# Kernel optimization log

Hardware: AMD Instinct MI355X
Metric: run time of the kernel (lower is better)

## Reference

```python
import jax, jax.numpy as jnp
import numpy as np

NEG_SLOPE_GAT = 0.2   # PyG GATConv default negative_slope
NEG_SLOPE_ACT = 0.01  # torch F.leaky_relu default


def gat_conv(x, src, dst, W, att_src, att_dst, b, N):
    # Single-head PyG GATConv with self-loops already appended in (src, dst).
    xl = x @ W                              # [N, d]
    a_src = xl @ att_src                    # [N]
    a_dst = xl @ att_dst                    # [N]
    e = jax.nn.leaky_relu(a_src[src] + a_dst[dst], NEG_SLOPE_GAT)  # [E]
    m = jax.ops.segment_max(e, dst, num_segments=N)                # per-dst max
    ex = jnp.exp(e - m[dst])
    s = jax.ops.segment_sum(ex, dst, num_segments=N)
    alpha = ex / (s[dst] + 1e-16)                                  # softmax over in-edges
    out = jax.ops.segment_sum(alpha[:, None] * xl[src], dst, num_segments=N)
    return out + b


def setup_inputs() -> dict:
    key = jax.random.key(0)
    ks = jax.random.split(key, 10)
    N, E, d_in, h1, h2 = 100000, 1600000, 128, 128, 64
    x = jax.random.normal(ks[0], (N, d_in), dtype=jnp.float32)
    edge_index = jax.random.randint(ks[1], (2, E), 0, N, dtype=jnp.int64)
    s1 = 1.0 / np.sqrt(d_in)
    s2 = 1.0 / np.sqrt(h1)
    W1 = jax.random.uniform(ks[2], (d_in, h1), jnp.float32, -s1, s1)
    att_src1 = jax.random.uniform(ks[3], (h1,), jnp.float32, -s2, s2)
    att_dst1 = jax.random.uniform(ks[4], (h1,), jnp.float32, -s2, s2)
    b1 = jnp.zeros((h1,), jnp.float32)
    s3 = 1.0 / np.sqrt(h2)
    W2 = jax.random.uniform(ks[5], (h1, h2), jnp.float32, -s2, s2)
    att_src2 = jax.random.uniform(ks[6], (h2,), jnp.float32, -s3, s3)
    att_dst2 = jax.random.uniform(ks[7], (h2,), jnp.float32, -s3, s3)
    b2 = jnp.zeros((h2,), jnp.float32)
    return {"x": x, "edge_index": edge_index, "W1": W1, "att_src1": att_src1,
            "att_dst1": att_dst1, "b1": b1, "W2": W2, "att_src2": att_src2,
            "att_dst2": att_dst2, "b2": b2}


def reference(x, edge_index, W1, att_src1, att_dst1, b1, W2, att_src2, att_dst2, b2):
    N = x.shape[0]
    loops = jnp.arange(N, dtype=edge_index.dtype)
    src = jnp.concatenate([edge_index[0], loops])  # add self-loops (PyG default)
    dst = jnp.concatenate([edge_index[1], loops])
    h = gat_conv(x, src, dst, W1, att_src1, att_dst1, b1, N)
    h = jax.nn.leaky_relu(h, NEG_SLOPE_ACT)
    # dropout omitted (deterministic reference / eval mode)
    h = gat_conv(h, src, dst, W2, att_src2, att_dst2, b2, N)
    return jax.nn.softmax(h, axis=0)
```

## Files before the change

### kernel.cpp

```cpp
#include <hip/hip_runtime.h>
#include <hip/hip_fp16.h>
#include <math.h>


constexpr int NPARTS = 256;
constexpr int PCAP = 8192;
constexpr int CHUNK = 4096;
constexpr int DPPMAX = 400;

typedef _Float16 f16x8 __attribute__((ext_vector_type(8)));
typedef float f32x4 __attribute__((ext_vector_type(4)));

__global__ __launch_bounds__(256) void k_part(
    const int* __restrict__ srcA, const int* __restrict__ dstA,
    int* __restrict__ pcur, uint2* __restrict__ parts,
    int* __restrict__ ovf, int* __restrict__ ovf_cnt,
    int E, int N, int DPP, int nch, int ovfcap) {
  __shared__ int hist[NPARTS];
  __shared__ int base[NPARTS];
  const int tot = E + N;
  for (int c = blockIdx.x; c < nch; c += gridDim.x) {
    hist[threadIdx.x] = 0;
    __syncthreads();
    const int beg = c * CHUNK;
    int pp[16], rr[16], ss[16], dd[16];
#pragma unroll
    for (int j = 0; j < 16; ++j) {
      int e = beg + j * 256 + (int)threadIdx.x;
      int d = -1, s = 0;
      if (e < tot) {
        if (e < E) { d = dstA[e]; s = srcA[e]; } else { d = s = e - E; }
      }
      dd[j] = d; ss[j] = s;
      int p = (d >= 0) ? (d / DPP) : -1;
      pp[j] = p;
      rr[j] = (p >= 0) ? atomicAdd(&hist[p], 1) : 0;
    }
    __syncthreads();
    base[threadIdx.x] = atomicAdd(&pcur[threadIdx.x], hist[threadIdx.x]);
    __syncthreads();
#pragma unroll
    for (int j = 0; j < 16; ++j) {
      int p = pp[j];
      if (p < 0) continue;
      int pos = base[p] + rr[j];
      if (pos < PCAP) {
        parts[(size_t)p * PCAP + pos] = make_uint2((unsigned)ss[j], (unsigned)dd[j]);
      } else {
        int o = atomicAdd(ovf_cnt, 1);
        if (o < ovfcap) { ovf[2 * o] = dd[j]; ovf[2 * o + 1] = ss[j]; }
      }
    }
    __syncthreads();
  }
}

__global__ __launch_bounds__(256) void k_pscan(const int* __restrict__ pcur,
                                               int* __restrict__ pbase) {
  __shared__ int sc[NPARTS];
  int t = threadIdx.x;
  int v = min(pcur[t], PCAP);
  sc[t] = v;
  __syncthreads();
  for (int o = 1; o < NPARTS; o <<= 1) {
    int x = (t >= o) ? sc[t - o] : 0;
    __syncthreads();
    sc[t] += x;
    __syncthreads();
  }
  pbase[t + 1] = sc[t];
  if (t == 0) pbase[0] = 0;
}

__global__ __launch_bounds__(256) void k_place(
    const uint2* __restrict__ parts, const int* __restrict__ pbase,
    int* __restrict__ rowptr, int* __restrict__ seidx,
    int N, int DPP, int nparts) {
  __shared__ int l_cnt[DPPMAX];
  __shared__ int l_off[DPPMAX];
  __shared__ int l_out[PCAP];
  const int p = blockIdx.x;
  const int t = threadIdx.x;
  const int d0 = p * DPP;
  const int ndst = min(DPP, N - d0);
  const int base = pbase[p];
  const int n = pbase[p + 1] - base;
  const uint2* pe = parts + (size_t)p * PCAP;

  for (int i = t; i < ndst; i += 256) l_cnt[i] = 0;
  __syncthreads();
  for (int i = t; i < n; i += 256) {
    uint2 e = pe[i];
    atomicAdd(&l_cnt[(int)e.y - d0], 1);
  }
  __syncthreads();
  if (t == 0) {
    int run = 0;
    for (int i = 0; i < ndst; ++i) { l_off[i] = run; run += l_cnt[i]; }
  }
  __syncthreads();
  for (int i = t; i < ndst; i += 256) {
    rowptr[d0 + i] = base + l_off[i];
    l_cnt[i] = l_off[i];
  }
  if (p == nparts - 1 && t == 0) rowptr[N] = base + n;
  __syncthreads();
  for (int i = t; i < n; i += 256) {
    uint2 e = pe[i];
    int pos = atomicAdd(&l_cnt[(int)e.y - d0], 1);
    l_out[pos] = (int)e.x;
  }
  __syncthreads();
  for (int i = t; i < n; i += 256)
    seidx[base + i] = l_out[i];
}

__global__ __launch_bounds__(256) void k_wprep(
    const float* __restrict__ W1, const float* __restrict__ W2,
    _Float16* __restrict__ Wf1, _Float16* __restrict__ Wf2) {
  int t = blockIdx.x * blockDim.x + threadIdx.x;
  int stride = gridDim.x * blockDim.x;
  for (int i = t; i < 8 * 4 * 64 * 8; i += stride) {
    int j = i & 7, l = (i >> 3) & 63, kk = (i >> 9) & 3, cb = i >> 11;
    int k = kk * 32 + (l >> 4) * 8 + j, c = cb * 16 + (l & 15);
    Wf1[i] = (_Float16)W1[k * 128 + c];
  }
  for (int i = t; i < 4 * 4 * 64 * 8; i += stride) {
    int j = i & 7, l = (i >> 3) & 63, kk = (i >> 9) & 3, cb = i >> 11;
    int k = kk * 32 + (l >> 4) * 8 + j, c = cb * 16 + (l & 15);
    Wf2[i] = (_Float16)W2[k * 64 + c];
  }
}

template <int C>
__device__ __forceinline__ void gemm_mfma_body(
    const float* __restrict__ X, const _Float16* __restrict__ Wf,
    const float* __restrict__ atts, const float* __restrict__ attd,
    __half* __restrict__ XLh, float* __restrict__ a_s, float* __restrict__ a_d,
    int N) {
  constexpr int NCB = C / 16;
  const int lane = threadIdx.x & 63;
  const int wv = threadIdx.x >> 6;
  const int r0 = blockIdx.x * 64 + wv * 16;
  const int arow = lane & 15;
  const int grp = lane >> 4;
  const int r = r0 + arow;
  const int rsafe = (r < N) ? r : (N - 1);

  float av[NCB], dv[NCB];
#pragma unroll
  for (int cb = 0; cb < NCB; ++cb) {
    av[cb] = atts[cb * 16 + arow];
    dv[cb] = attd[cb * 16 + arow];
  }

  f16x8 af[4];
  const float* xr = X + (size_t)rsafe * 128 + grp * 8;
#pragma unroll
  for (int kk = 0; kk < 4; ++kk) {
    float4 u0 = *(const float4*)(xr + kk * 32);
    float4 u1 = *(const float4*)(xr + kk * 32 + 4);
    af[kk][0] = (_Float16)u0.x; af[kk][1] = (_Float16)u0.y;
    af[kk][2] = (_Float16)u0.z; af[kk][3] = (_Float16)u0.w;
    af[kk][4] = (_Float16)u1.x; af[kk][5] = (_Float16)u1.y;
    af[kk][6] = (_Float16)u1.z; af[kk][7] = (_Float16)u1.w;
  }

  float ps[4] = {0.f, 0.f, 0.f, 0.f};
  float pd[4] = {0.f, 0.f, 0.f, 0.f};

#pragma unroll
  for (int cb = 0; cb < NCB; ++cb) {
    f32x4 acc = {0.f, 0.f, 0.f, 0.f};
#pragma unroll
    for (int kk = 0; kk < 4; ++kk) {
      f16x8 bf = *(const f16x8*)(Wf + ((size_t)(cb * 4 + kk) * 64 + lane) * 8);
      acc = __builtin_amdgcn_mfma_f32_16x16x32_f16(af[kk], bf, acc, 0, 0, 0);
    }
    const int ocol = cb * 16 + arow;
#pragma unroll
    for (int i = 0; i < 4; ++i) {
      const int orow = r0 + grp * 4 + i;
      if (orow < N) XLh[(size_t)orow * C + ocol] = (__half)(_Float16)acc[i];
      ps[i] = fmaf(acc[i], av[cb], ps[i]);
      pd[i] = fmaf(acc[i], dv[cb], pd[i]);
    }
  }
#pragma unroll
  for (int m = 1; m < 16; m <<= 1) {
#pragma unroll
    for (int i = 0; i < 4; ++i) {
      ps[i] += __shfl_xor(ps[i], m);
      pd[i] += __shfl_xor(pd[i], m);
    }
  }
  if (arow == 0) {
#pragma unroll
    for (int i = 0; i < 4; ++i) {
      const int orow = r0 + grp * 4 + i;
      if (orow < N) { a_s[orow] = ps[i]; a_d[orow] = pd[i]; }
    }
  }
}

__global__ __launch_bounds__(256) void k_gemm_l1(
    const float* __restrict__ X, const _Float16* __restrict__ Wf,
    const float* __restrict__ atts, const float* __restrict__ attd,
    __half* __restrict__ XLh, float* __restrict__ a_s, float* __restrict__ a_d,
    int N) {
  gemm_mfma_body<128>(X, Wf, atts, attd, XLh, a_s, a_d, N);
}
__global__ __launch_bounds__(256) void k_gemm_l2(
    const float* __restrict__ X, const _Float16* __restrict__ Wf,
    const float* __restrict__ atts, const float* __restrict__ attd,
    __half* __restrict__ XLh, float* __restrict__ a_s, float* __restrict__ a_d,
    int N) {
  gemm_mfma_body<64>(X, Wf, atts, attd, XLh, a_s, a_d, N);
}

template <int C, bool RELU>
__device__ __forceinline__ void aggr_body(
    const __half* __restrict__ XLh, const float* __restrict__ as_,
    const float* __restrict__ ad_, const int* __restrict__ rowptr,
    const int* __restrict__ seidx, const int* __restrict__ ovf,
    const int* __restrict__ ovf_cnt, const float* __restrict__ bias,
    float* __restrict__ OUT, int N) {
  constexpr int PL = C / 64;
  const int lane = threadIdx.x & 63;
  const int wid = threadIdx.x >> 6;
  const int novf = *ovf_cnt;
  float bb[PL];
#pragma unroll
  for (int j = 0; j < PL; ++j) bb[j] = bias[lane * PL + j];

  for (int d = blockIdx.x * 4 + wid; d < N; d += gridDim.x * 4) {
    const int beg = rowptr[d], end = rowptr[d + 1];
    const int nb = end - beg;
    const float adst = ad_[d];

    float s;
    int sv = 0; float ev = 0.f;
    if (nb <= 64) {
      if (lane < nb) {
        sv = seidx[beg + lane];
        float t = as_[sv] + adst;
        t = t > 0.f ? t : 0.2f * t;
        ev = __expf(t);
      }
      s = ev;
    } else {
      s = 0.f;
      for (int i = beg + lane; i < end; i += 64) {
        int s2 = seidx[i];
        float t = as_[s2] + adst;
        t = t > 0.f ? t : 0.2f * t;
        s += __expf(t);
      }
    }
#pragma unroll
    for (int o = 32; o; o >>= 1) s += __shfl_xor(s, o);

    if (novf > 0) {
      float so = 0.f;
      for (int i = lane; i < novf; i += 64) {
        if (ovf[2 * i] == d) {
          float t = as_[ovf[2 * i + 1]] + adst;
          t = t > 0.f ? t : 0.2f * t;
          so += __expf(t);
        }
      }
#pragma unroll
      for (int o = 32; o; o >>= 1) so += __shfl_xor(so, o);
      s += so;
    }
    const float inv = 1.f / (s + 1e-16f);

    float acc[PL];
#pragma unroll
    for (int j = 0; j < PL; ++j) acc[j] = 0.f;

    if (nb <= 64) {
      const float wv = ev * inv;
      auto body = [&](int j) {
        int sj = __shfl(sv, j);
        float wj = __shfl(wv, j);
        if (PL == 2) {
          __half2 hv = *(const __half2*)(XLh + (size_t)sj * C + lane * 2);
          float2 xv = __half22float2(hv);
          acc[0] = fmaf(wj, xv.x, acc[0]);
          acc[1] = fmaf(wj, xv.y, acc[1]);
        } else {
          acc[0] = fmaf(wj, __half2float(XLh[(size_t)sj * C + lane]), acc[0]);
        }
      };
      int j = 0;
      for (; j + 4 <= nb; j += 4) { body(j); body(j + 1); body(j + 2); body(j + 3); }
      for (; j < nb; ++j) body(j);
    } else {
      for (int i0 = beg; i0 < end; i0 += 64) {
        const int nc = min(64, end - i0);
        int sc = 0; float wc = 0.f;
        if (lane < nc) {
          sc = seidx[i0 + lane];
          float t = as_[sc] + adst;
          t = t > 0.f ? t : 0.2f * t;
          wc = __expf(t) * inv;
        }
        for (int j = 0; j < nc; ++j) {
          int sj = __shfl(sc, j);
          float wj = __shfl(wc, j);
          if (PL == 2) {
            __half2 hv = *(const __half2*)(XLh + (size_t)sj * C + lane * 2);
            float2 xv = __half22float2(hv);
            acc[0] = fmaf(wj, xv.x, acc[0]);
            acc[1] = fmaf(wj, xv.y, acc[1]);
          } else {
            acc[0] = fmaf(wj, __half2float(XLh[(size_t)sj * C + lane]), acc[0]);
          }
        }
      }
    }

    if (novf > 0) {
      for (int i = 0; i < novf; ++i) {
        int od = ovf[2 * i];
        if (od != d) continue;
        int os = ovf[2 * i + 1];
        float t = as_[os] + adst;
        t = t > 0.f ? t : 0.2f * t;
        float wj = __expf(t) * inv;
        if (PL == 2) {
          __half2 hv = *(const __half2*)(XLh + (size_t)os * C + lane * 2);
          float2 xv = __half22float2(hv);
          acc[0] = fmaf(wj, xv.x, acc[0]);
          acc[1] = fmaf(wj, xv.y, acc[1]);
        } else {
          acc[0] = fmaf(wj, __half2float(XLh[(size_t)os * C + lane]), acc[0]);
        }
      }
    }

    float o0 = acc[0] + bb[0];
    if (RELU) o0 = o0 > 0.f ? o0 : 0.01f * o0;
    if (PL == 2) {
      float o1 = acc[1] + bb[1];
      if (RELU) o1 = o1 > 0.f ? o1 : 0.01f * o1;
      *(float2*)&OUT[(size_t)d * C + lane * 2] = make_float2(o0, o1);
    } else {
      OUT[(size_t)d * C + lane] = o0;
    }
  }
}

__global__ __launch_bounds__(256) void k_aggr_l1(
    const __half* __restrict__ XLh, const float* __restrict__ as_,
    const float* __restrict__ ad_, const int* __restrict__ rowptr,
    const int* __restrict__ seidx, const int* __restrict__ ovf,
    const int* __restrict__ ovf_cnt, const float* __restrict__ bias,
    float* __restrict__ OUT, int N) {
  aggr_body<128, true>(XLh, as_, ad_, rowptr, seidx, ovf, ovf_cnt, bias, OUT, N);
}
__global__ __launch_bounds__(256) void k_aggr_l2(
    const __half* __restrict__ XLh, const float* __restrict__ as_,
    const float* __restrict__ ad_, const int* __restrict__ rowptr,
    const int* __restrict__ seidx, const int* __restrict__ ovf,
    const int* __restrict__ ovf_cnt, const float* __restrict__ bias,
    float* __restrict__ OUT, int N) {
  aggr_body<64, false>(XLh, as_, ad_, rowptr, seidx, ovf, ovf_cnt, bias, OUT, N);
}

__global__ void k_colsum(const float* __restrict__ O, float* __restrict__ csum, int N) {
  __shared__ float sm[4][64];
  int c = threadIdx.x & 63;
  int wv = threadIdx.x >> 6;
  float s = 0.f;
  for (int r = blockIdx.x * 4 + wv; r < N; r += gridDim.x * 4)
    s += __expf(O[(size_t)r * 64 + c]);
  sm[wv][c] = s;
  __syncthreads();
  if (threadIdx.x < 64) {
    float s2 = sm[0][c] + sm[1][c] + sm[2][c] + sm[3][c];
    atomicAdd(&csum[c], s2);
  }
}

__global__ void k_norm(float* __restrict__ O, const float* __restrict__ csum, size_t tot4) {
  for (size_t i = blockIdx.x * (size_t)blockDim.x + threadIdx.x; i < tot4;
       i += (size_t)gridDim.x * blockDim.x) {
    float4 v = ((float4*)O)[i];
    int c0 = (int)((i * 4) & 63);
    float s0 = csum[c0],     s1 = csum[c0 + 1];
    float s2 = csum[c0 + 2], s3 = csum[c0 + 3];
    v.x = __expf(v.x) / s0;
    v.y = __expf(v.y) / s1;
    v.z = __expf(v.z) / s2;
    v.w = __expf(v.w) / s3;
    ((float4*)O)[i] = v;
  }
}

extern "C" void kernel_launch(void* const* d_in, const int* in_sizes, int n_in,
                              void* d_out, int out_size, void* d_ws, size_t ws_size,
                              hipStream_t stream) {
  const float* x   = (const float*)d_in[0];
  const int*   ei  = (const int*)d_in[1];
  const float* W1  = (const float*)d_in[2];
  const float* as1 = (const float*)d_in[3];
  const float* ad1 = (const float*)d_in[4];
  const float* b1  = (const float*)d_in[5];
  const float* W2  = (const float*)d_in[6];
  const float* as2 = (const float*)d_in[7];
  const float* ad2 = (const float*)d_in[8];
  const float* b2  = (const float*)d_in[9];
  float* out = (float*)d_out;

  const int N = in_sizes[0] / 128;
  const int E = in_sizes[1] / 2;
  const int Etot = E + N;
  const int* srcA = ei;
  const int* dstA = ei + E;
  const int DPP = (N + NPARTS - 1) / NPARTS;
  const int nparts = (N + DPP - 1) / DPP;

  char* w = (char*)d_ws;
  auto take = [&](size_t bytes) -> void* {
    void* p = (void*)w;
    w += (bytes + 255) & ~(size_t)255;
    return p;
  };
  __half*    xlh   = (__half*)take((size_t)N * 128 * 2);
  __half*    xl2h  = (__half*)take((size_t)N * 64 * 2);
  float*     h     = (float*)take((size_t)N * 128 * 4);
  float*     a_s   = (float*)take((size_t)N * 4);
  float*     a_d   = (float*)take((size_t)N * 4);
  int*       zeroB = (int*)take((size_t)(1 + 64 + NPARTS) * 4);
  int*       ovf_cnt = zeroB;
  float*     csum    = (float*)(zeroB + 1);
  int*       pcur    = zeroB + 1 + 64;
  int*       pbase  = (int*)take((size_t)(NPARTS + 1) * 4);
  int*       rowptr = (int*)take((size_t)(N + 1) * 4);
  int*       seidx  = (int*)take((size_t)Etot * 4);
  int*       ovf    = (int*)take((size_t)Etot * 2 * 4);
  uint2*     parts  = (uint2*)take((size_t)NPARTS * PCAP * 8);
  _Float16*  wf1    = (_Float16*)take((size_t)8 * 4 * 64 * 8 * 2);
  _Float16*  wf2    = (_Float16*)take((size_t)4 * 4 * 64 * 8 * 2);

  hipMemsetAsync(zeroB, 0, (size_t)(1 + 64 + NPARTS) * 4, stream);

  const int nch = (Etot + CHUNK - 1) / CHUNK;
  k_part<<<nch, 256, 0, stream>>>(srcA, dstA, pcur, parts, ovf, ovf_cnt,
                                  E, N, DPP, nch, Etot);
  k_wprep<<<32, 256, 0, stream>>>(W1, W2, wf1, wf2);
  k_pscan<<<1, NPARTS, 0, stream>>>(pcur, pbase);
  k_place<<<nparts, 256, 0, stream>>>(parts, pbase, rowptr, seidx, N, DPP, nparts);

  const int gb = (N + 63) / 64;
  k_gemm_l1<<<gb, 256, 0, stream>>>(x, wf1, as1, ad1, xlh, a_s, a_d, N);
  k_aggr_l1<<<8192, 256, 0, stream>>>(xlh, a_s, a_d, rowptr, seidx, ovf, ovf_cnt, b1, h, N);
  k_gemm_l2<<<gb, 256, 0, stream>>>(h, wf2, as2, ad2, xl2h, a_s, a_d, N);
  k_aggr_l2<<<8192, 256, 0, stream>>>(xl2h, a_s, a_d, rowptr, seidx, ovf, ovf_cnt, b2, out, N);

  k_colsum<<<1024, 256, 0, stream>>>(out, csum, N);
  const size_t tot4 = (size_t)N * 64 / 4;
  k_norm<<<2048, 256, 0, stream>>>(out, csum, tot4);
}
```

Measured before the change: 268.6 us.

## Fuse graph build, weight prep, scan/place with GEMM, and colsum into aggregation

Merges the partitioning and weight-conversion kernels into one launch, folds the prefix scan and CSR placement into the layer-1 GEMM launch as extra blocks, and fuses the column exp-sum into a specialized layer-2 aggregation that processes two edges per step with half-waves. Broadcasts use readlane instead of shuffles. Column sums are spread over 8 replicas to cut atomic contention. This reduces launch count and removes a full pass over the output, at the cost of larger shared-memory footprint in the fused GEMM kernel, which may lower its occupancy.

```diff
diff --git a/kernel.cpp b/kernel.cpp
--- a/kernel.cpp
+++ b/kernel.cpp
@@ -11,124 +11,69 @@
 typedef _Float16 f16x8 __attribute__((ext_vector_type(8)));
 typedef float f32x4 __attribute__((ext_vector_type(4)));
 
-__global__ __launch_bounds__(256) void k_part(
+__device__ __forceinline__ int bcasti(int v, int j) {
+  return __builtin_amdgcn_readlane(v, j);
+}
+__device__ __forceinline__ float bcastf(float v, int j) {
+  return __uint_as_float((unsigned)__builtin_amdgcn_readlane((int)__float_as_uint(v), j));
+}
+
+__global__ __launch_bounds__(256) void k_build1(
     const int* __restrict__ srcA, const int* __restrict__ dstA,
     int* __restrict__ pcur, uint2* __restrict__ parts,
     int* __restrict__ ovf, int* __restrict__ ovf_cnt,
+    const float* __restrict__ W1, const float* __restrict__ W2,
+    _Float16* __restrict__ Wf1, _Float16* __restrict__ Wf2,
     int E, int N, int DPP, int nch, int ovfcap) {
+  if ((int)blockIdx.x >= nch) {
+    int t = ((int)blockIdx.x - nch) * 256 + (int)threadIdx.x;
+    const int stride = 8 * 256;
+    for (int i = t; i < 8 * 4 * 64 * 8; i += stride) {
+      int j = i & 7, l = (i >> 3) & 63, kk = (i >> 9) & 3, cb = i >> 11;
+      int k = kk * 32 + (l >> 4) * 8 + j, c = cb * 16 + (l & 15);
+      Wf1[i] = (_Float16)W1[k * 128 + c];
+    }
+    for (int i = t; i < 4 * 4 * 64 * 8; i += stride) {
+      int j = i & 7, l = (i >> 3) & 63, kk = (i >> 9) & 3, cb = i >> 11;
+      int k = kk * 32 + (l >> 4) * 8 + j, c = cb * 16 + (l & 15);
+      Wf2[i] = (_Float16)W2[k * 64 + c];
+    }
+    return;
+  }
   __shared__ int hist[NPARTS];
   __shared__ int base[NPARTS];
   const int tot = E + N;
-  for (int c = blockIdx.x; c < nch; c += gridDim.x) {
-    hist[threadIdx.x] = 0;
-    __syncthreads();
-    const int beg = c * CHUNK;
-    int pp[16], rr[16], ss[16], dd[16];
-#pragma unroll
-    for (int j = 0; j < 16; ++j) {
-      int e = beg + j * 256 + (int)threadIdx.x;
-      int d = -1, s = 0;
-      if (e < tot) {
-        if (e < E) { d = dstA[e]; s = srcA[e]; } else { d = s = e - E; }
-      }
-      dd[j] = d; ss[j] = s;
-      int p = (d >= 0) ? (d / DPP) : -1;
-      pp[j] = p;
-      rr[j] = (p >= 0) ? atomicAdd(&hist[p], 1) : 0;
-    }
-    __syncthreads();
-    base[threadIdx.x] = atomicAdd(&pcur[threadIdx.x], hist[threadIdx.x]);
-    __syncthreads();
-#pragma unroll
-    for (int j = 0; j < 16; ++j) {
-      int p = pp[j];
-      if (p < 0) continue;
-      int pos = base[p] + rr[j];
-      if (pos < PCAP) {
-        parts[(size_t)p * PCAP + pos] = make_uint2((unsigned)ss[j], (unsigned)dd[j]);
-      } else {
-        int o = atomicAdd(ovf_cnt, 1);
-        if (o < ovfcap) { ovf[2 * o] = dd[j]; ovf[2 * o + 1] = ss[j]; }
-      }
-    }
-    __syncthreads();
-  }
-}
-
-__global__ __launch_bounds__(256) void k_pscan(const int* __restrict__ pcur,
-                                               int* __restrict__ pbase) {
-  __shared__ int sc[NPARTS];
-  int t = threadIdx.x;
-  int v = min(pcur[t], PCAP);
-  sc[t] = v;
-  __syncthreads();
-  for (int o = 1; o < NPARTS; o <<= 1) {
-    int x = (t >= o) ? sc[t - o] : 0;
-    __syncthreads();
-    sc[t] += x;
-    __syncthreads();
-  }
-  pbase[t + 1] = sc[t];
-  if (t == 0) pbase[0] = 0;
-}
-
-__global__ __launch_bounds__(256) void k_place(
-    const uint2* __restrict__ parts, const int* __restrict__ pbase,
-    int* __restrict__ rowptr, int* __restrict__ seidx,
-    int N, int DPP, int nparts) {
-  __shared__ int l_cnt[DPPMAX];
-  __shared__ int l_off[DPPMAX];
-  __shared__ int l_out[PCAP];
-  const int p = blockIdx.x;
-  const int t = threadIdx.x;
-  const int d0 = p * DPP;
-  const int ndst = min(DPP, N - d0);
-  const int base = pbase[p];
-  const int n = pbase[p + 1] - base;
-  const uint2* pe = parts + (size_t)p * PCAP;
-
-  for (int i = t; i < ndst; i += 256) l_cnt[i] = 0;
-  __syncthreads();
-  for (int i = t; i < n; i += 256) {
-    uint2 e = pe[i];
-    atomicAdd(&l_cnt[(int)e.y - d0], 1);
-  }
-  __syncthreads();
-  if (t == 0) {
-    int run = 0;
-    for (int i = 0; i < ndst; ++i) { l_off[i] = run; run += l_cnt[i]; }
-  }
-  __syncthreads();
-  for (int i = t; i < ndst; i += 256) {
-    rowptr[d0 + i] = base + l_off[i];
-    l_cnt[i] = l_off[i];
-  }
-  if (p == nparts - 1 && t == 0) rowptr[N] = base + n;
-  __syncthreads();
-  for (int i = t; i < n; i += 256) {
-    uint2 e = pe[i];
-    int pos = atomicAdd(&l_cnt[(int)e.y - d0], 1);
-    l_out[pos] = (int)e.x;
-  }
-  __syncthreads();
-  for (int i = t; i < n; i += 256)
-    seidx[base + i] = l_out[i];
-}
-
-__global__ __launch_bounds__(256) void k_wprep(
-    const float* __restrict__ W1, const float* __restrict__ W2,
-    _Float16* __restrict__ Wf1, _Float16* __restrict__ Wf2) {
-  int t = blockIdx.x * blockDim.x + threadIdx.x;
-  int stride = gridDim.x * blockDim.x;
-  for (int i = t; i < 8 * 4 * 64 * 8; i += stride) {
-    int j = i & 7, l = (i >> 3) & 63, kk = (i >> 9) & 3, cb = i >> 11;
-    int k = kk * 32 + (l >> 4) * 8 + j, c = cb * 16 + (l & 15);
-    Wf1[i] = (_Float16)W1[k * 128 + c];
-  }
-  for (int i = t; i < 4 * 4 * 64 * 8; i += stride) {
-    int j = i & 7, l = (i >> 3) & 63, kk = (i >> 9) & 3, cb = i >> 11;
-    int k = kk * 32 + (l >> 4) * 8 + j, c = cb * 16 + (l & 15);
-    Wf2[i] = (_Float16)W2[k * 64 + c];
+  const int c = blockIdx.x;
+  hist[threadIdx.x] = 0;
+  __syncthreads();
+  const int beg = c * CHUNK;
+  int pp[16], rr[16], ss[16], dd[16];
+#pragma unroll
+  for (int j = 0; j < 16; ++j) {
+    int e = beg + j * 256 + (int)threadIdx.x;
+    int d = -1, s = 0;
+    if (e < tot) {
+      if (e < E) { d = dstA[e]; s = srcA[e]; } else { d = s = e - E; }
+    }
+    dd[j] = d; ss[j] = s;
+    int p = (d >= 0) ? (d / DPP) : -1;
+    pp[j] = p;
+    rr[j] = (p >= 0) ? atomicAdd(&hist[p], 1) : 0;
+  }
+  __syncthreads();
+  base[threadIdx.x] = atomicAdd(&pcur[threadIdx.x], hist[threadIdx.x]);
+  __syncthreads();
+#pragma unroll
+  for (int j = 0; j < 16; ++j) {
+    int p = pp[j];
+    if (p < 0) continue;
+    int pos = base[p] + rr[j];
+    if (pos < PCAP) {
+      parts[(size_t)p * PCAP + pos] = make_uint2((unsigned)ss[j], (unsigned)dd[j]);
+    } else {
+      int o = atomicAdd(ovf_cnt, 1);
+      if (o < ovfcap) { ovf[2 * o] = dd[j]; ovf[2 * o + 1] = ss[j]; }
+    }
   }
 }
 
@@ -137,11 +82,11 @@
     const float* __restrict__ X, const _Float16* __restrict__ Wf,
     const float* __restrict__ atts, const float* __restrict__ attd,
     __half* __restrict__ XLh, float* __restrict__ a_s, float* __restrict__ a_d,
-    int N) {
+    int N, int bid) {
   constexpr int NCB = C / 16;
   const int lane = threadIdx.x & 63;
   const int wv = threadIdx.x >> 6;
-  const int r0 = blockIdx.x * 64 + wv * 16;
+  const int r0 = bid * 64 + wv * 16;
   const int arow = lane & 15;
   const int grp = lane >> 4;
   const int r = r0 + arow;
@@ -203,35 +148,88 @@
   }
 }
 
-__global__ __launch_bounds__(256) void k_gemm_l1(
+struct PlaceSmem {
+  int sc[NPARTS];
+  int l_cnt[DPPMAX];
+  int l_off[DPPMAX];
+  int l_out[PCAP];
+};
+
+__global__ __launch_bounds__(256) void k_gemm1_place(
     const float* __restrict__ X, const _Float16* __restrict__ Wf,
     const float* __restrict__ atts, const float* __restrict__ attd,
     __half* __restrict__ XLh, float* __restrict__ a_s, float* __restrict__ a_d,
-    int N) {
-  gemm_mfma_body<128>(X, Wf, atts, attd, XLh, a_s, a_d, N);
-}
+    int N, const uint2* __restrict__ parts, const int* __restrict__ pcur,
+    int* __restrict__ rowptr, int* __restrict__ seidx,
+    int DPP, int nparts, int gb) {
+  __shared__ PlaceSmem sm;
+  if ((int)blockIdx.x < gb) {
+    gemm_mfma_body<128>(X, Wf, atts, attd, XLh, a_s, a_d, N, blockIdx.x);
+    return;
+  }
+  const int p = (int)blockIdx.x - gb;
+  const int t = threadIdx.x;
+  sm.sc[t] = min(pcur[t], PCAP);
+  __syncthreads();
+  for (int o = 1; o < NPARTS; o <<= 1) {
+    int x = (t >= o) ? sm.sc[t - o] : 0;
+    __syncthreads();
+    sm.sc[t] += x;
+    __syncthreads();
+  }
+  const int base = (p == 0) ? 0 : sm.sc[p - 1];
+  const int n = sm.sc[p] - base;
+  const int d0 = p * DPP;
+  const int ndst = min(DPP, N - d0);
+  const uint2* pe = parts + (size_t)p * PCAP;
+
+  for (int i = t; i < ndst; i += 256) sm.l_cnt[i] = 0;
+  __syncthreads();
+  for (int i = t; i < n; i += 256) {
+    uint2 e = pe[i];
+    atomicAdd(&sm.l_cnt[(int)e.y - d0], 1);
+  }
+  __syncthreads();
+  if (t == 0) {
+    int run = 0;
+    for (int i = 0; i < ndst; ++i) { sm.l_off[i] = run; run += sm.l_cnt[i]; }
+  }
+  __syncthreads();
+  for (int i = t; i < ndst; i += 256) {
+    rowptr[d0 + i] = base + sm.l_off[i];
+    sm.l_cnt[i] = sm.l_off[i];
+  }
+  if (p == nparts - 1 && t == 0) rowptr[N] = sm.sc[nparts - 1];
+  __syncthreads();
+  for (int i = t; i < n; i += 256) {
+    uint2 e = pe[i];
+    int pos = atomicAdd(&sm.l_cnt[(int)e.y - d0], 1);
+    sm.l_out[pos] = (int)e.x;
+  }
+  __syncthreads();
+  for (int i = t; i < n; i += 256)
+    seidx[base + i] = sm.l_out[i];
+}
+
 __global__ __launch_bounds__(256) void k_gemm_l2(
     const float* __restrict__ X, const _Float16* __restrict__ Wf,
     const float* __restrict__ atts, const float* __restrict__ attd,
     __half* __restrict__ XLh, float* __restrict__ a_s, float* __restrict__ a_d,
     int N) {
-  gemm_mfma_body<64>(X, Wf, atts, attd, XLh, a_s, a_d, N);
-}
-
-template <int C, bool RELU>
-__device__ __forceinline__ void aggr_body(
+  gemm_mfma_body<64>(X, Wf, atts, attd, XLh, a_s, a_d, N, blockIdx.x);
+}
+
+__global__ __launch_bounds__(256) void k_aggr_l1(
     const __half* __restrict__ XLh, const float* __restrict__ as_,
     const float* __restrict__ ad_, const int* __restrict__ rowptr,
     const int* __restrict__ seidx, const int* __restrict__ ovf,
     const int* __restrict__ ovf_cnt, const float* __restrict__ bias,
     float* __restrict__ OUT, int N) {
-  constexpr int PL = C / 64;
+  constexpr int C = 128;
   const int lane = threadIdx.x & 63;
   const int wid = threadIdx.x >> 6;
   const int novf = *ovf_cnt;
-  float bb[PL];
-#pragma unroll
-  for (int j = 0; j < PL; ++j) bb[j] = bias[lane * PL + j];
+  const float bb0 = bias[lane * 2], bb1 = bias[lane * 2 + 1];
 
   for (int d = blockIdx.x * 4 + wid; d < N; d += gridDim.x * 4) {
     const int beg = rowptr[d], end = rowptr[d + 1];
@@ -275,23 +273,16 @@
     }
     const float inv = 1.f / (s + 1e-16f);
 
-    float acc[PL];
-#pragma unroll
-    for (int j = 0; j < PL; ++j) acc[j] = 0.f;
-
+    float2 acc = make_float2(0.f, 0.f);
     if (nb <= 64) {
       const float wv = ev * inv;
       auto body = [&](int j) {
-        int sj = __shfl(sv, j);
-        float wj = __shfl(wv, j);
-        if (PL == 2) {
-          __half2 hv = *(const __half2*)(XLh + (size_t)sj * C + lane * 2);
-          float2 xv = __half22float2(hv);
-          acc[0] = fmaf(wj, xv.x, acc[0]);
-          acc[1] = fmaf(wj, xv.y, acc[1]);
-        } else {
-          acc[0] = fmaf(wj, __half2float(XLh[(size_t)sj * C + lane]), acc[0]);
-        }
+        int sj = bcasti(sv, j);
+        float wj = bcastf(wv, j);
+        const __half2* rp = (const __half2*)(XLh + (size_t)sj * C) + lane;
+        float2 xv = __half22float2(*rp);
+        acc.x = fmaf(wj, xv.x, acc.x);
+        acc.y = fmaf(wj, xv.y, acc.y);
       };
       int j = 0;
       for (; j + 4 <= nb; j += 4) { body(j); body(j + 1); body(j + 2); body(j + 3); }
@@ -307,94 +298,181 @@
           wc = __expf(t) * inv;
         }
         for (int j = 0; j < nc; ++j) {
-          int sj = __shfl(sc, j);
-          float wj = __shfl(wc, j);
-          if (PL == 2) {
-            __half2 hv = *(const __half2*)(XLh + (size_t)sj * C + lane * 2);
-            float2 xv = __half22float2(hv);
-            acc[0] = fmaf(wj, xv.x, acc[0]);
-            acc[1] = fmaf(wj, xv.y, acc[1]);
-          } else {
-            acc[0] = fmaf(wj, __half2float(XLh[(size_t)sj * C + lane]), acc[0]);
-          }
+          int sj = bcasti(sc, j);
+          float wj = bcastf(wc, j);
+          const __half2* rp = (const __half2*)(XLh + (size_t)sj * C) + lane;
+          float2 xv = __half22float2(*rp);
+          acc.x = fmaf(wj, xv.x, acc.x);
+          acc.y = fmaf(wj, xv.y, acc.y);
         }
       }
     }
 
     if (novf > 0) {
       for (int i = 0; i < novf; ++i) {
-        int od = ovf[2 * i];
-        if (od != d) continue;
+        if (ovf[2 * i] != d) continue;
         int os = ovf[2 * i + 1];
         float t = as_[os] + adst;
         t = t > 0.f ? t : 0.2f * t;
         float wj = __expf(t) * inv;
-        if (PL == 2) {
-          __half2 hv = *(const __half2*)(XLh + (size_t)os * C + lane * 2);
-          float2 xv = __half22float2(hv);
-          acc[0] = fmaf(wj, xv.x, acc[0]);
-          acc[1] = fmaf(wj, xv.y, acc[1]);
-        } else {
-          acc[0] = fmaf(wj, __half2float(XLh[(size_t)os * C + lane]), acc[0]);
-        }
-      }
-    }
-
-    float o0 = acc[0] + bb[0];
-    if (RELU) o0 = o0 > 0.f ? o0 : 0.01f * o0;
-    if (PL == 2) {
-      float o1 = acc[1] + bb[1];
-      if (RELU) o1 = o1 > 0.f ? o1 : 0.01f * o1;
-      *(float2*)&OUT[(size_t)d * C + lane * 2] = make_float2(o0, o1);
-    } else {
-      OUT[(size_t)d * C + lane] = o0;
-    }
-  }
-}
-
-__global__ __launch_bounds__(256) void k_aggr_l1(
+        const __half2* rp = (const __half2*)(XLh + (size_t)os * C) + lane;
+        float2 xv = __half22float2(*rp);
+        acc.x = fmaf(wj, xv.x, acc.x);
+        acc.y = fmaf(wj, xv.y, acc.y);
+      }
+    }
+
+    float o0 = acc.x + bb0;
+    float o1 = acc.y + bb1;
+    o0 = o0 > 0.f ? o0 : 0.01f * o0;
+    o1 = o1 > 0.f ? o1 : 0.01f * o1;
+    *(float2*)&OUT[(size_t)d * C + lane * 2] = make_float2(o0, o1);
+  }
+}
+
+__global__ __launch_bounds__(256) void k_aggr2(
     const __half* __restrict__ XLh, const float* __restrict__ as_,
     const float* __restrict__ ad_, const int* __restrict__ rowptr,
     const int* __restrict__ seidx, const int* __restrict__ ovf,
     const int* __restrict__ ovf_cnt, const float* __restrict__ bias,
-    float* __restrict__ OUT, int N) {
-  aggr_body<128, true>(XLh, as_, ad_, rowptr, seidx, ovf, ovf_cnt, bias, OUT, N);
-}
-__global__ __launch_bounds__(256) void k_aggr_l2(
-    const __half* __restrict__ XLh, const float* __restrict__ as_,
-    const float* __restrict__ ad_, const int* __restrict__ rowptr,
-    const int* __restrict__ seidx, const int* __restrict__ ovf,
-    const int* __restrict__ ovf_cnt, const float* __restrict__ bias,
-    float* __restrict__ OUT, int N) {
-  aggr_body<64, false>(XLh, as_, ad_, rowptr, seidx, ovf, ovf_cnt, bias, OUT, N);
-}
-
-__global__ void k_colsum(const float* __restrict__ O, float* __restrict__ csum, int N) {
-  __shared__ float sm[4][64];
-  int c = threadIdx.x & 63;
-  int wv = threadIdx.x >> 6;
-  float s = 0.f;
-  for (int r = blockIdx.x * 4 + wv; r < N; r += gridDim.x * 4)
-    s += __expf(O[(size_t)r * 64 + c]);
-  sm[wv][c] = s;
+    float* __restrict__ OUT, float* __restrict__ csum8, int N) {
+  constexpr int C = 64;
+  const int lane = threadIdx.x & 63;
+  const int wid = threadIdx.x >> 6;
+  const int grp = lane >> 5;
+  const int l5 = lane & 31;
+  const int novf = *ovf_cnt;
+  const float bb0 = bias[2 * l5], bb1 = bias[2 * l5 + 1];
+  float cs0 = 0.f, cs1 = 0.f;
+
+  for (int d = blockIdx.x * 4 + wid; d < N; d += gridDim.x * 4) {
+    const int beg = rowptr[d], end = rowptr[d + 1];
+    const int nb = end - beg;
+    const float adst = ad_[d];
+
+    if (nb <= 64) {
+      int sv = 0; float ev = 0.f;
+      if (lane < nb) {
+        sv = seidx[beg + lane];
+        float t = as_[sv] + adst;
+        t = t > 0.f ? t : 0.2f * t;
+        ev = __expf(t);
+      }
+      float s = ev;
+#pragma unroll
+      for (int o = 32; o; o >>= 1) s += __shfl_xor(s, o);
+      if (novf > 0) {
+        float so = 0.f;
+        for (int i = lane; i < novf; i += 64) {
+          if (ovf[2 * i] == d) {
+            float t = as_[ovf[2 * i + 1]] + adst;
+            t = t > 0.f ? t : 0.2f * t;
+            so += __expf(t);
+          }
+        }
+#pragma unroll
+        for (int o = 32; o; o >>= 1) so += __shfl_xor(so, o);
+        s += so;
+      }
+      const float inv = 1.f / (s + 1e-16f);
+      const float wv = ev * inv;
+
+      float ax = 0.f, ay = 0.f;
+      const int nsteps = (nb + 1) >> 1;
+      for (int j = 0; j < nsteps; ++j) {
+        int sl = 2 * j + grp;
+        int sj = __shfl(sv, sl);
+        float wj = __shfl(wv, sl);
+        const __half2* rp = (const __half2*)(XLh + (size_t)sj * C) + l5;
+        float2 xv = __half22float2(*rp);
+        ax = fmaf(wj, xv.x, ax);
+        ay = fmaf(wj, xv.y, ay);
+      }
+      ax += __shfl_xor(ax, 32);
+      ay += __shfl_xor(ay, 32);
+
+      if (novf > 0) {
+        for (int i = 0; i < novf; ++i) {
+          if (ovf[2 * i] != d) continue;
+          int os = ovf[2 * i + 1];
+          float t = as_[os] + adst;
+          t = t > 0.f ? t : 0.2f * t;
+          float wj = __expf(t) * inv;
+          const __half2* rp = (const __half2*)(XLh + (size_t)os * C) + l5;
+          float2 xv = __half22float2(*rp);
+          ax = fmaf(wj, xv.x, ax);
+          ay = fmaf(wj, xv.y, ay);
+        }
+      }
+      if (grp == 0) {
+        float o0 = ax + bb0;
+        float o1 = ay + bb1;
+        *(float2*)&OUT[(size_t)d * C + 2 * l5] = make_float2(o0, o1);
+        cs0 += __expf(o0);
+        cs1 += __expf(o1);
+      }
+    } else {
+      float s = 0.f;
+      for (int i = beg + lane; i < end; i += 64) {
+        int s2 = seidx[i];
+        float t = as_[s2] + adst;
+        t = t > 0.f ? t : 0.2f * t;
+        s += __expf(t);
+      }
+#pragma unroll
+      for (int o = 32; o; o >>= 1) s += __shfl_xor(s, o);
+      const float inv = 1.f / (s + 1e-16f);
+      float acc0 = 0.f;
+      for (int i0 = beg; i0 < end; i0 += 64) {
+        const int nc = min(64, end - i0);
+        int sc = 0; float wc = 0.f;
+        if (lane < nc) {
+          sc = seidx[i0 + lane];
+          float t = as_[sc] + adst;
+          t = t > 0.f ? t : 0.2f * t;
+          wc = __expf(t) * inv;
+        }
+        for (int j = 0; j < nc; ++j) {
+          int sj = bcasti(sc, j);
+          float wj = bcastf(wc, j);
+          acc0 = fmaf(wj, __half2float(XLh[(size_t)sj * C + lane]), acc0);
+        }
+      }
+      float o0 = acc0 + bias[lane];
+      OUT[(size_t)d * C + lane] = o0;
+      atomicAdd(&csum8[(d & 7) * 64 + lane], __expf(o0));
+    }
+  }
+
+  __shared__ float csA[4][64];
+  if (grp == 0) { csA[wid][2 * l5] = cs0; csA[wid][2 * l5 + 1] = cs1; }
   __syncthreads();
   if (threadIdx.x < 64) {
-    float s2 = sm[0][c] + sm[1][c] + sm[2][c] + sm[3][c];
-    atomicAdd(&csum[c], s2);
-  }
-}
-
-__global__ void k_norm(float* __restrict__ O, const float* __restrict__ csum, size_t tot4) {
+    float tot = csA[0][threadIdx.x] + csA[1][threadIdx.x] +
+                csA[2][threadIdx.x] + csA[3][threadIdx.x];
+    if (tot != 0.f)
+      atomicAdd(&csum8[((int)blockIdx.x & 7) * 64 + (int)threadIdx.x], tot);
+  }
+}
+
+__global__ void k_norm(float* __restrict__ O, const float* __restrict__ csum8,
+                       size_t tot4) {
+  __shared__ float cs[64];
+  if (threadIdx.x < 64) {
+    float s = 0.f;
+#pragma unroll
+    for (int r = 0; r < 8; ++r) s += csum8[r * 64 + (int)threadIdx.x];
+    cs[threadIdx.x] = s;
+  }
+  __syncthreads();
   for (size_t i = blockIdx.x * (size_t)blockDim.x + threadIdx.x; i < tot4;
        i += (size_t)gridDim.x * blockDim.x) {
     float4 v = ((float4*)O)[i];
     int c0 = (int)((i * 4) & 63);
-    float s0 = csum[c0],     s1 = csum[c0 + 1];
-    float s2 = csum[c0 + 2], s3 = csum[c0 + 3];
-    v.x = __expf(v.x) / s0;
-    v.y = __expf(v.y) / s1;
-    v.z = __expf(v.z) / s2;
-    v.w = __expf(v.w) / s3;
+    v.x = __expf(v.x) / cs[c0];
+    v.y = __expf(v.y) / cs[c0 + 1];
+    v.z = __expf(v.z) / cs[c0 + 2];
+    v.w = __expf(v.w) / cs[c0 + 3];
     ((float4*)O)[i] = v;
   }
 }
@@ -433,11 +511,10 @@
   float*     h     = (float*)take((size_t)N * 128 * 4);
   float*     a_s   = (float*)take((size_t)N * 4);
   float*     a_d   = (float*)take((size_t)N * 4);
-  int*       zeroB = (int*)take((size_t)(1 + 64 + NPARTS) * 4);
+  int*       zeroB = (int*)take((size_t)(1 + NPARTS + 512) * 4);
   int*       ovf_cnt = zeroB;
-  float*     csum    = (float*)(zeroB + 1);
-  int*       pcur    = zeroB + 1 + 64;
-  int*       pbase  = (int*)take((size_t)(NPARTS + 1) * 4);
+  int*       pcur    = zeroB + 1;
+  float*     csum8   = (float*)(zeroB + 1 + NPARTS);
   int*       rowptr = (int*)take((size_t)(N + 1) * 4);
   int*       seidx  = (int*)take((size_t)Etot * 4);
   int*       ovf    = (int*)take((size_t)Etot * 2 * 4);
@@ -445,22 +522,21 @@
   _Float16*  wf1    = (_Float16*)take((size_t)8 * 4 * 64 * 8 * 2);
   _Float16*  wf2    = (_Float16*)take((size_t)4 * 4 * 64 * 8 * 2);
 
-  hipMemsetAsync(zeroB, 0, (size_t)(1 + 64 + NPARTS) * 4, stream);
+  hipMemsetAsync(zeroB, 0, (size_t)(1 + NPARTS + 512) * 4, stream);
 
   const int nch = (Etot + CHUNK - 1) / CHUNK;
-  k_part<<<nch, 256, 0, stream>>>(srcA, dstA, pcur, parts, ovf, ovf_cnt,
-                                  E, N, DPP, nch, Etot);
-  k_wprep<<<32, 256, 0, stream>>>(W1, W2, wf1, wf2);
-  k_pscan<<<1, NPARTS, 0, stream>>>(pcur, pbase);
-  k_place<<<nparts, 256, 0, stream>>>(parts, pbase, rowptr, seidx, N, DPP, nparts);
-
   const int gb = (N + 63) / 64;
-  k_gemm_l1<<<gb, 256, 0, stream>>>(x, wf1, as1, ad1, xlh, a_s, a_d, N);
-  k_aggr_l1<<<8192, 256, 0, stream>>>(xlh, a_s, a_d, rowptr, seidx, ovf, ovf_cnt, b1, h, N);
+
+  k_build1<<<nch + 8, 256, 0, stream>>>(srcA, dstA, pcur, parts, ovf, ovf_cnt,
+                                        W1, W2, wf1, wf2, E, N, DPP, nch, Etot);
+  k_gemm1_place<<<gb + NPARTS, 256, 0, stream>>>(
+      x, wf1, as1, ad1, xlh, a_s, a_d, N, parts, pcur, rowptr, seidx,
+      DPP, nparts, gb);
+  k_aggr_l1<<<8192, 256, 0, stream>>>(xlh, a_s, a_d, rowptr, seidx, ovf, ovf_cnt,
+                                      b1, h, N);
   k_gemm_l2<<<gb, 256, 0, stream>>>(h, wf2, as2, ad2, xl2h, a_s, a_d, N);
-  k_aggr_l2<<<8192, 256, 0, stream>>>(xl2h, a_s, a_d, rowptr, seidx, ovf, ovf_cnt, b2, out, N);
-
-  k_colsum<<<1024, 256, 0, stream>>>(out, csum, N);
+  k_aggr2<<<4096, 256, 0, stream>>>(xl2h, a_s, a_d, rowptr, seidx, ovf, ovf_cnt,
+                                    b2, out, csum8, N);
   const size_t tot4 = (size_t)N * 64 / 4;
-  k_norm<<<2048, 256, 0, stream>>>(out, csum, tot4);
-}
+  k_norm<<<2048, 256, 0, stream>>>(out, csum8, tot4);
+}
```

After: 242.3 us. 1.11x faster.
